# Kernel tuning notes

Hardware: AMD Instinct MI355X
Metric: run time of the kernel (lower is better)

The kernel has to match this reference:

```python
import jax, jax.numpy as jnp
import numpy as np

N, E = 50000, 800000
IN_C, HID, HEADS, OUT_C = 128, 256, 4, 40
C1 = HID // HEADS  # 64 per-head channels in layer 1
NEG_SLOPE = 0.2


def gat_conv(x, edge_index, W, att_src, att_dst, bias, heads, ch, concat):
    """PyG-style GATConv (inference). W:[heads*ch,in], att_*:[heads,ch], bias matches output."""
    n = x.shape[0]
    loop = jnp.arange(n, dtype=edge_index.dtype)
    src = jnp.concatenate([edge_index[0], loop])  # add self-loops (PyG default)
    dst = jnp.concatenate([edge_index[1], loop])
    h = (x @ W.T).reshape(n, heads, ch)                       # [N,H,C]
    a_src = jnp.einsum('nhc,hc->nh', h, att_src)              # [N,H]
    a_dst = jnp.einsum('nhc,hc->nh', h, att_dst)
    logits = jax.nn.leaky_relu(a_src[src] + a_dst[dst], NEG_SLOPE)  # [E',H]
    m = jax.lax.stop_gradient(jax.ops.segment_max(logits, dst, num_segments=n))
    e = jnp.exp(logits - m[dst])
    denom = jax.ops.segment_sum(e, dst, num_segments=n)
    alpha = e / (denom[dst] + 1e-16)                          # [E',H]
    msg = h[src] * alpha[:, :, None]                          # [E',H,C]
    out = jax.ops.segment_sum(msg, dst, num_segments=n)       # [N,H,C]
    out = out.reshape(n, heads * ch) if concat else out.mean(axis=1)
    return out + bias


def setup_inputs() -> dict:
    key = jax.random.key(0)
    ks = jax.random.split(key, 10)
    x = jax.random.normal(ks[0], (N, IN_C), dtype=jnp.float32)
    edge_index = jax.random.randint(ks[1], (2, E), 0, N, dtype=jnp.int64)
    s = 0.1
    W1 = jax.random.normal(ks[2], (HEADS * C1, IN_C), dtype=jnp.float32) * s
    att_src1 = jax.random.normal(ks[3], (HEADS, C1), dtype=jnp.float32) * s
    att_dst1 = jax.random.normal(ks[4], (HEADS, C1), dtype=jnp.float32) * s
    b1 = jnp.zeros((HEADS * C1,), dtype=jnp.float32)
    W2 = jax.random.normal(ks[5], (OUT_C, HID), dtype=jnp.float32) * s
    att_src2 = jax.random.normal(ks[6], (1, OUT_C), dtype=jnp.float32) * s
    att_dst2 = jax.random.normal(ks[7], (1, OUT_C), dtype=jnp.float32) * s
    b2 = jnp.zeros((OUT_C,), dtype=jnp.float32)
    return {"x": x, "edge_index": edge_index, "W1": W1, "att_src1": att_src1,
            "att_dst1": att_dst1, "b1": b1, "W2": W2, "att_src2": att_src2,
            "att_dst2": att_dst2, "b2": b2}


def reference(x, edge_index, W1, att_src1, att_dst1, b1, W2, att_src2, att_dst2, b2):
    h = gat_conv(x, edge_index, W1, att_src1, att_dst1, b1, HEADS, C1, True)
    h = jax.nn.elu(h)
    out = gat_conv(h, edge_index, W2, att_src2, att_dst2, b2, 1, OUT_C, False)
    return out
```

## Files before the change

kernel.cpp:

```cpp
#include <hip/hip_runtime.h>
#include <hip/hip_bf16.h>
#include <cstdint>
#include <cstddef>

#define NN 50000
#define NE 800000
#define INC 128
#define HIDC 256
#define NH 4
#define OUTC 40

#define GE_BLOCKS ((NE + 255)/256)
#define CVT_BLOCKS ((HIDC*INC/4 + 255)/256)
#define G1_BLOCKS ((NN + 63)/64)

typedef __attribute__((ext_vector_type(8))) short short8_t;
typedef __attribute__((ext_vector_type(4))) float f32x4_t;

__device__ __forceinline__ float lrelu(float x){ return x > 0.f ? x : 0.2f*x; }
__device__ __forceinline__ unsigned short bfr(float f){
  __hip_bfloat16 h = __float2bfloat16(f);
  return *reinterpret_cast<unsigned short*>(&h);
}
__device__ __forceinline__ float bflo(unsigned u){ return __uint_as_float(u << 16); }
__device__ __forceinline__ float bfhi(unsigned u){ return __uint_as_float(u & 0xffff0000u); }

__device__ __forceinline__ int probe_flag(const void* ei, int tid, int* sflag){
  if (tid < 64){
    long long v = ((const long long*)ei)[(long long)tid * (NE/64)];
    bool ok = (v >= 0) && (v < NN);
    unsigned long long m = __ballot(ok);
    if (tid == 0) *sflag = (m == 0xFFFFFFFFFFFFFFFFull) ? 1 : 0;
  }
  __syncthreads();
  return *sflag;
}

__global__ __launch_bounds__(256) void k_count_cvt(const void* __restrict__ ei, int* __restrict__ deg,
                                                   const float* __restrict__ W1, unsigned short* __restrict__ w1b){
  int tid = threadIdx.x;
  if (blockIdx.x < CVT_BLOCKS){
    int i = blockIdx.x*256 + tid;
    if (i < HIDC*INC/4){
      float4 v = ((const float4*)W1)[i];
      ushort4 o;
      o.x = bfr(v.x); o.y = bfr(v.y); o.z = bfr(v.z); o.w = bfr(v.w);
      ((ushort4*)w1b)[i] = o;
    }
    return;
  }
  __shared__ int sflag;
  int flag = probe_flag(ei, tid, &sflag);
  int e = (blockIdx.x - CVT_BLOCKS)*256 + tid;
  if (e >= NE) return;
  int d;
  if (flag) d = (int)((const long long*)ei)[NE+e];
  else      d = ((const int*)ei)[NE+e];
  d = min(max(d,0),NN-1);
  atomicAdd(&deg[d], 1);
}

__global__ __launch_bounds__(1024) void k_scan1(const int* __restrict__ deg, int* __restrict__ rowptr, int* __restrict__ sums){
  __shared__ int sh[1024];
  int t = threadIdx.x; int i = blockIdx.x*1024 + t;
  sh[t] = (i < NN) ? deg[i] : 0;
  __syncthreads();
  for (int off = 1; off < 1024; off <<= 1){
    int add = (t >= off) ? sh[t-off] : 0;
    __syncthreads();
    sh[t] += add;
    __syncthreads();
  }
  if (i < NN) rowptr[i+1] = sh[t];
  if (t == 1023) sums[blockIdx.x] = sh[1023];
}

__global__ __launch_bounds__(256) void k_scan3(int* __restrict__ rowptr, const int* __restrict__ sums, int nchunks){
  __shared__ int spre[64];
  int t = threadIdx.x;
  if (t == 0){
    int acc = 0;
    for (int c = 0; c < nchunks; c++){ spre[c] = acc; acc += sums[c]; }
  }
  __syncthreads();
  int i = blockIdx.x*256 + t;
  if (i < NN) rowptr[i+1] += spre[i >> 10];
  if (i == 0) rowptr[0] = 0;
}

__global__ __launch_bounds__(256) void k_gemm1_fill(const float* __restrict__ x, const unsigned short* __restrict__ w1b,
    const float* __restrict__ atts, const float* __restrict__ attd,
    unsigned short* __restrict__ h1b, float* __restrict__ as1, float* __restrict__ ad1,
    const void* __restrict__ ei, const int* __restrict__ rowptr, int* __restrict__ fillc,
    int* __restrict__ colsrc){
  int tid = threadIdx.x;
  if (blockIdx.x < G1_BLOCKS){
    int wv = tid >> 6, l = tid & 63;
    int m0 = blockIdx.x*64 + wv*16;
    int lr = l & 15;
    int lk = l >> 4;

    short8_t a[4];
    int arow = m0 + lr; if (arow > NN-1) arow = NN-1;
    const float* xrow = x + (size_t)arow*INC + lk*8;
    #pragma unroll
    for (int kt = 0; kt < 4; kt++){
      float4 f0 = *(const float4*)(xrow + kt*32);
      float4 f1 = *(const float4*)(xrow + kt*32 + 4);
      short8_t av;
      av[0] = (short)bfr(f0.x); av[1] = (short)bfr(f0.y);
      av[2] = (short)bfr(f0.z); av[3] = (short)bfr(f0.w);
      av[4] = (short)bfr(f1.x); av[5] = (short)bfr(f1.y);
      av[6] = (short)bfr(f1.z); av[7] = (short)bfr(f1.w);
      a[kt] = av;
    }

    const unsigned short* bbase = w1b + (size_t)lr*INC + lk*8;

    for (int h = 0; h < NH; h++){
      float ps[4] = {0.f,0.f,0.f,0.f};
      float pd[4] = {0.f,0.f,0.f,0.f};
      #pragma unroll
      for (int t4 = 0; t4 < 4; t4++){
        int nt = h*4 + t4;
        f32x4_t acc = {0.f,0.f,0.f,0.f};
        #pragma unroll
        for (int kt = 0; kt < 4; kt++){
          short8_t bv = *(const short8_t*)(bbase + (size_t)nt*16*INC + kt*32);
          acc = __builtin_amdgcn_mfma_f32_16x16x32_bf16(a[kt], bv, acc, 0, 0, 0);
        }
        float sa = atts[nt*16 + lr], sd = attd[nt*16 + lr];
        #pragma unroll
        for (int r = 0; r < 4; r++){
          float v = acc[r];
          ps[r] += v*sa; pd[r] += v*sd;
          int node = m0 + lk*4 + r;
          if (node < NN) h1b[(size_t)node*HIDC + nt*16 + lr] = bfr(v);
        }
      }
      #pragma unroll
      for (int r = 0; r < 4; r++){
        float p = ps[r], q = pd[r];
        p += __shfl_xor(p, 1); p += __shfl_xor(p, 2); p += __shfl_xor(p, 4); p += __shfl_xor(p, 8);
        q += __shfl_xor(q, 1); q += __shfl_xor(q, 2); q += __shfl_xor(q, 4); q += __shfl_xor(q, 8);
        int node = m0 + lk*4 + r;
        if (lr == 0 && node < NN){ as1[node*NH + h] = p; ad1[node*NH + h] = q; }
      }
    }
    return;
  }
  __shared__ int sflag;
  int flag = probe_flag(ei, tid, &sflag);
  int e = (blockIdx.x - G1_BLOCKS)*256 + tid;
  if (e >= NE) return;
  int s, d;
  if (flag){
    const long long* p = (const long long*)ei;
    s = (int)p[e]; d = (int)p[NE+e];
  } else {
    const int* p = (const int*)ei;
    s = p[e]; d = p[NE+e];
  }
  s = min(max(s,0),NN-1); d = min(max(d,0),NN-1);
  int pos = rowptr[d] + atomicAdd(&fillc[d], 1);
  colsrc[pos] = s;
}

__global__ __launch_bounds__(128) void k_agg1(const unsigned short* __restrict__ h1b,
    const float* __restrict__ as1, const float* __restrict__ ad1,
    const int* __restrict__ colsrc, const int* __restrict__ rowptr,
    const float* __restrict__ b1, unsigned short* __restrict__ h1a){
  int n = blockIdx.x*2 + (threadIdx.x >> 6);
  if (n >= NN) return;
  int tid = threadIdx.x & 63;
  int head = tid >> 4;
  const uint2* h1q = (const uint2*)h1b;

  float adn = ad1[n*NH + head];
  float es_self = __expf(lrelu(as1[n*NH + head] + adn));
  float den = 1e-16f + es_self;
  uint2 v = h1q[(size_t)n*64 + tid];
  float a0 = es_self * bflo(v.x);
  float a1 = es_self * bfhi(v.x);
  float a2 = es_self * bflo(v.y);
  float a3 = es_self * bfhi(v.y);

  int beg = rowptr[n], end = rowptr[n+1];
  int j = beg;
  for (; j + 7 < end; j += 8){
    int s[8]; float w[8]; uint2 g[8];
    #pragma unroll
    for (int u = 0; u < 8; u++) s[u] = colsrc[j+u];
    #pragma unroll
    for (int u = 0; u < 8; u++) g[u] = h1q[(size_t)s[u]*64 + tid];
    #pragma unroll
    for (int u = 0; u < 8; u++) w[u] = as1[s[u]*NH + head];
    #pragma unroll
    for (int u = 0; u < 8; u++) w[u] = __expf(lrelu(w[u] + adn));
    #pragma unroll
    for (int u = 0; u < 8; u++){
      den += w[u];
      a0 += w[u]*bflo(g[u].x); a1 += w[u]*bfhi(g[u].x);
      a2 += w[u]*bflo(g[u].y); a3 += w[u]*bfhi(g[u].y);
    }
  }
  for (; j + 3 < end; j += 4){
    int s[4]; float w[4]; uint2 g[4];
    #pragma unroll
    for (int u = 0; u < 4; u++) s[u] = colsrc[j+u];
    #pragma unroll
    for (int u = 0; u < 4; u++) g[u] = h1q[(size_t)s[u]*64 + tid];
    #pragma unroll
    for (int u = 0; u < 4; u++) w[u] = __expf(lrelu(as1[s[u]*NH + head] + adn));
    #pragma unroll
    for (int u = 0; u < 4; u++){
      den += w[u];
      a0 += w[u]*bflo(g[u].x); a1 += w[u]*bfhi(g[u].x);
      a2 += w[u]*bflo(g[u].y); a3 += w[u]*bfhi(g[u].y);
    }
  }
  for (; j < end; j++){
    int s0 = colsrc[j];
    uint2 g0 = h1q[(size_t)s0*64 + tid];
    float w0 = __expf(lrelu(as1[s0*NH + head] + adn));
    den += w0;
    a0 += w0*bflo(g0.x); a1 += w0*bfhi(g0.x); a2 += w0*bflo(g0.y); a3 += w0*bfhi(g0.y);
  }

  float4 bb = ((const float4*)b1)[tid];
  float rinv = 1.f / den;
  float o0 = a0*rinv + bb.x;
  float o1 = a1*rinv + bb.y;
  float o2 = a2*rinv + bb.z;
  float o3 = a3*rinv + bb.w;
  o0 = o0 > 0.f ? o0 : (__expf(o0) - 1.f);
  o1 = o1 > 0.f ? o1 : (__expf(o1) - 1.f);
  o2 = o2 > 0.f ? o2 : (__expf(o2) - 1.f);
  o3 = o3 > 0.f ? o3 : (__expf(o3) - 1.f);
  uint2 pkd;
  pkd.x = (unsigned)bfr(o0) | ((unsigned)bfr(o1) << 16);
  pkd.y = (unsigned)bfr(o2) | ((unsigned)bfr(o3) << 16);
  ((uint2*)h1a)[(size_t)n*64 + tid] = pkd;
}

__global__ __launch_bounds__(128) void k_gemm2(const unsigned short* __restrict__ h1a, const float* __restrict__ W2,
    const float* __restrict__ atts2, const float* __restrict__ attd2,
    unsigned* __restrict__ h2b, float* __restrict__ a2s, float* __restrict__ a2d){
  __shared__ float W2t[HIDC*OUTC];
  __shared__ float sA[OUTC], sD[OUTC];
  int tid = threadIdx.x;
  #pragma unroll
  for (int it = 0; it < (OUTC*HIDC)/128; it++){
    int idx = it*128 + tid;
    int c = idx >> 8, k = idx & 255;
    W2t[k*OUTC + c] = W2[idx];
  }
  if (tid < OUTC){ sA[tid] = atts2[tid]; sD[tid] = attd2[tid]; }
  __syncthreads();

  int n = blockIdx.x*128 + tid;
  if (n >= NN) return;

  float acc[OUTC];
  #pragma unroll
  for (int c = 0; c < OUTC; c++) acc[c] = 0.f;

  const uint2* x2p = (const uint2*)(h1a + (size_t)n*HIDC);
  const float4* w4p = (const float4*)W2t;
  #pragma unroll 2
  for (int k4 = 0; k4 < HIDC/4; k4++){
    uint2 xu = x2p[k4];
    float xk[4] = { bflo(xu.x), bfhi(xu.x), bflo(xu.y), bfhi(xu.y) };
    #pragma unroll
    for (int kk = 0; kk < 4; kk++){
      #pragma unroll
      for (int c4 = 0; c4 < OUTC/4; c4++){
        float4 wv = w4p[(k4*4 + kk)*(OUTC/4) + c4];
        acc[c4*4+0] += xk[kk]*wv.x;
        acc[c4*4+1] += xk[kk]*wv.y;
        acc[c4*4+2] += xk[kk]*wv.z;
        acc[c4*4+3] += xk[kk]*wv.w;
      }
    }
  }

  float s2 = 0.f, d2 = 0.f;
  #pragma unroll
  for (int c = 0; c < OUTC; c++){ s2 += acc[c]*sA[c]; d2 += acc[c]*sD[c]; }

  unsigned* h2row = h2b + (size_t)n*(OUTC/2);
  #pragma unroll
  for (int c2 = 0; c2 < OUTC/2; c2++)
    h2row[c2] = (unsigned)bfr(acc[c2*2]) | ((unsigned)bfr(acc[c2*2+1]) << 16);
  a2s[n] = s2; a2d[n] = d2;
}

__global__ __launch_bounds__(128) void k_agg2(const unsigned* __restrict__ h2b, const float* __restrict__ a2s,
    const float* __restrict__ a2d, const int* __restrict__ colsrc, const int* __restrict__ rowptr,
    const float* __restrict__ b2, float* __restrict__ out){
  int tid = threadIdx.x & 63;
  int half = threadIdx.x >> 6;
  int sub = tid / 20, c2 = tid % 20;
  int n = blockIdx.x*6 + half*3 + sub;
  bool valid = (sub < 3) && (n < NN);
  int nn = valid ? n : 0;

  float a2dn = a2d[nn];
  float e = __expf(lrelu(a2s[nn] + a2dn));
  float den = 1e-16f + e;
  unsigned v = h2b[(size_t)nn*20 + c2];
  float acc0 = e * bflo(v);
  float acc1 = e * bfhi(v);

  int beg = valid ? rowptr[nn] : 0;
  int end = valid ? rowptr[nn+1] : 0;
  int j = beg;
  for (; j + 7 < end; j += 8){
    int s[8]; float w[8]; unsigned g[8];
    #pragma unroll
    for (int u = 0; u < 8; u++) s[u] = colsrc[j+u];
    #pragma unroll
    for (int u = 0; u < 8; u++) g[u] = h2b[(size_t)s[u]*20 + c2];
    #pragma unroll
    for (int u = 0; u < 8; u++) w[u] = a2s[s[u]];
    #pragma unroll
    for (int u = 0; u < 8; u++) w[u] = __expf(lrelu(w[u] + a2dn));
    #pragma unroll
    for (int u = 0; u < 8; u++){
      den += w[u];
      acc0 += w[u]*bflo(g[u]);
      acc1 += w[u]*bfhi(g[u]);
    }
  }
  for (; j + 3 < end; j += 4){
    int s[4]; float w[4]; unsigned g[4];
    #pragma unroll
    for (int u = 0; u < 4; u++) s[u] = colsrc[j+u];
    #pragma unroll
    for (int u = 0; u < 4; u++) g[u] = h2b[(size_t)s[u]*20 + c2];
    #pragma unroll
    for (int u = 0; u < 4; u++) w[u] = __expf(lrelu(a2s[s[u]] + a2dn));
    #pragma unroll
    for (int u = 0; u < 4; u++){
      den += w[u];
      acc0 += w[u]*bflo(g[u]);
      acc1 += w[u]*bfhi(g[u]);
    }
  }
  for (; j < end; j++){
    int s0 = colsrc[j];
    unsigned g0 = h2b[(size_t)s0*20 + c2];
    float w0 = __expf(lrelu(a2s[s0] + a2dn));
    den += w0;
    acc0 += w0*bflo(g0);
    acc1 += w0*bfhi(g0);
  }

  if (valid){
    float rinv = 1.f / den;
    float2 o;
    o.x = acc0*rinv + b2[c2*2];
    o.y = acc1*rinv + b2[c2*2+1];
    ((float2*)(out + (size_t)n*OUTC))[c2] = o;
  }
}

extern "C" void kernel_launch(void* const* d_in, const int* in_sizes, int n_in,
                              void* d_out, int out_size, void* d_ws, size_t ws_size,
                              hipStream_t stream){
  const float* x    = (const float*)d_in[0];
  const void*  ei   = d_in[1];
  const float* W1   = (const float*)d_in[2];
  const float* as1w = (const float*)d_in[3];
  const float* ad1w = (const float*)d_in[4];
  const float* b1   = (const float*)d_in[5];
  const float* W2   = (const float*)d_in[6];
  const float* as2w = (const float*)d_in[7];
  const float* ad2w = (const float*)d_in[8];
  const float* b2   = (const float*)d_in[9];
  float* out = (float*)d_out;

  char* base = (char*)d_ws;
  size_t off = 0;
  auto alloc = [&](size_t bytes)->char*{ char* r = base + off; off += (bytes + 255) & ~(size_t)255; return r; };
  int* deg    = (int*)alloc((size_t)NN*sizeof(int));
  int* rowptr = (int*)alloc((size_t)(NN+1)*sizeof(int));
  int* fillc  = (int*)alloc((size_t)NN*sizeof(int));
  int* sums   = (int*)alloc(64*sizeof(int));
  int* colsrc = (int*)alloc((size_t)NE*sizeof(int));
  unsigned short* w1b = (unsigned short*)alloc((size_t)HIDC*INC*sizeof(unsigned short));
  unsigned short* h1b = (unsigned short*)alloc((size_t)NN*HIDC*sizeof(unsigned short));
  unsigned short* h1a = (unsigned short*)alloc((size_t)NN*HIDC*sizeof(unsigned short));
  float* as1  = (float*)alloc((size_t)NN*NH*sizeof(float));
  float* ad1  = (float*)alloc((size_t)NN*NH*sizeof(float));
  unsigned* h2b = (unsigned*)alloc((size_t)NN*(OUTC/2)*sizeof(unsigned));
  float* a2s  = (float*)alloc((size_t)NN*sizeof(float));
  float* a2d  = (float*)alloc((size_t)NN*sizeof(float));

  hipMemsetAsync(deg,   0, (size_t)NN*sizeof(int), stream);
  hipMemsetAsync(fillc, 0, (size_t)NN*sizeof(int), stream);

  int nchunks = (NN + 1023)/1024;
  k_count_cvt<<<CVT_BLOCKS + GE_BLOCKS, 256, 0, stream>>>(ei, deg, W1, w1b);
  k_scan1<<<nchunks, 1024, 0, stream>>>(deg, rowptr, sums);
  k_scan3<<<(NN + 255)/256, 256, 0, stream>>>(rowptr, sums, nchunks);
  k_gemm1_fill<<<G1_BLOCKS + GE_BLOCKS, 256, 0, stream>>>(x, w1b, as1w, ad1w, h1b, as1, ad1,
                                                          ei, rowptr, fillc, colsrc);
  k_agg1<<<(NN + 1)/2, 128, 0, stream>>>(h1b, as1, ad1, colsrc, rowptr, b1, h1a);
  k_gemm2<<<(NN + 127)/128, 128, 0, stream>>>(h1a, W2, as2w, ad2w, h2b, a2s, a2d);
  k_agg2<<<(NN + 5)/6, 128, 0, stream>>>(h2b, a2s, a2d, colsrc, rowptr, b2, out);
}
```

Before: 230.9 us.

## Split hidden features into 32-channel planes and slice aggregation across blocks

```diff
diff --git a/kernel.cpp b/kernel.cpp
--- a/kernel.cpp
+++ b/kernel.cpp
@@ -75,7 +75,8 @@
   if (t == 1023) sums[blockIdx.x] = sh[1023];
 }
 
-__global__ __launch_bounds__(256) void k_scan3(int* __restrict__ rowptr, const int* __restrict__ sums, int nchunks){
+__global__ __launch_bounds__(256) void k_scan3(int* __restrict__ rowptr, const int* __restrict__ sums, int nchunks,
+                                               int* __restrict__ fillc){
   __shared__ int spre[64];
   int t = threadIdx.x;
   if (t == 0){
@@ -84,13 +85,13 @@
   }
   __syncthreads();
   int i = blockIdx.x*256 + t;
-  if (i < NN) rowptr[i+1] += spre[i >> 10];
+  if (i < NN){ rowptr[i+1] += spre[i >> 10]; fillc[i] = 0; }
   if (i == 0) rowptr[0] = 0;
 }
 
 __global__ __launch_bounds__(256) void k_gemm1_fill(const float* __restrict__ x, const unsigned short* __restrict__ w1b,
     const float* __restrict__ atts, const float* __restrict__ attd,
-    unsigned short* __restrict__ h1b, float* __restrict__ as1, float* __restrict__ ad1,
+    unsigned short* __restrict__ h1p, float* __restrict__ as1, float* __restrict__ ad1,
     const void* __restrict__ ei, const int* __restrict__ rowptr, int* __restrict__ fillc,
     int* __restrict__ colsrc){
   int tid = threadIdx.x;
@@ -129,13 +130,15 @@
           short8_t bv = *(const short8_t*)(bbase + (size_t)nt*16*INC + kt*32);
           acc = __builtin_amdgcn_mfma_f32_16x16x32_bf16(a[kt], bv, acc, 0, 0, 0);
         }
-        float sa = atts[nt*16 + lr], sd = attd[nt*16 + lr];
+        int col = nt*16 + lr;
+        int plane = col >> 5, within = col & 31;
+        float sa = atts[col], sd = attd[col];
         #pragma unroll
         for (int r = 0; r < 4; r++){
           float v = acc[r];
           ps[r] += v*sa; pd[r] += v*sd;
           int node = m0 + lk*4 + r;
-          if (node < NN) h1b[(size_t)node*HIDC + nt*16 + lr] = bfr(v);
+          if (node < NN) h1p[(size_t)plane*NN*32 + (size_t)node*32 + within] = bfr(v);
         }
       }
       #pragma unroll
@@ -166,20 +169,23 @@
   colsrc[pos] = s;
 }
 
-__global__ __launch_bounds__(128) void k_agg1(const unsigned short* __restrict__ h1b,
+__global__ __launch_bounds__(128) void k_agg1(const unsigned short* __restrict__ h1p,
     const float* __restrict__ as1, const float* __restrict__ ad1,
     const int* __restrict__ colsrc, const int* __restrict__ rowptr,
     const float* __restrict__ b1, unsigned short* __restrict__ h1a){
-  int n = blockIdx.x*2 + (threadIdx.x >> 6);
+  int slice = blockIdx.x & 7;
+  int grp = blockIdx.x >> 3;
+  int n = grp*16 + (threadIdx.x >> 3);
   if (n >= NN) return;
-  int tid = threadIdx.x & 63;
-  int head = tid >> 4;
-  const uint2* h1q = (const uint2*)h1b;
+  int li = threadIdx.x & 7;
+  int head = slice >> 1;
+
+  const uint2* hp = (const uint2*)h1p + (size_t)slice*NN*8;
 
   float adn = ad1[n*NH + head];
   float es_self = __expf(lrelu(as1[n*NH + head] + adn));
   float den = 1e-16f + es_self;
-  uint2 v = h1q[(size_t)n*64 + tid];
+  uint2 v = hp[(size_t)n*8 + li];
   float a0 = es_self * bflo(v.x);
   float a1 = es_self * bfhi(v.x);
   float a2 = es_self * bflo(v.y);
@@ -187,31 +193,16 @@
 
   int beg = rowptr[n], end = rowptr[n+1];
   int j = beg;
-  for (; j + 7 < end; j += 8){
-    int s[8]; float w[8]; uint2 g[8];
-    #pragma unroll
-    for (int u = 0; u < 8; u++) s[u] = colsrc[j+u];
-    #pragma unroll
-    for (int u = 0; u < 8; u++) g[u] = h1q[(size_t)s[u]*64 + tid];
-    #pragma unroll
-    for (int u = 0; u < 8; u++) w[u] = as1[s[u]*NH + head];
-    #pragma unroll
-    for (int u = 0; u < 8; u++) w[u] = __expf(lrelu(w[u] + adn));
-    #pragma unroll
-    for (int u = 0; u < 8; u++){
-      den += w[u];
-      a0 += w[u]*bflo(g[u].x); a1 += w[u]*bfhi(g[u].x);
-      a2 += w[u]*bflo(g[u].y); a3 += w[u]*bfhi(g[u].y);
-    }
-  }
   for (; j + 3 < end; j += 4){
     int s[4]; float w[4]; uint2 g[4];
     #pragma unroll
     for (int u = 0; u < 4; u++) s[u] = colsrc[j+u];
     #pragma unroll
-    for (int u = 0; u < 4; u++) g[u] = h1q[(size_t)s[u]*64 + tid];
-    #pragma unroll
-    for (int u = 0; u < 4; u++) w[u] = __expf(lrelu(as1[s[u]*NH + head] + adn));
+    for (int u = 0; u < 4; u++) g[u] = hp[(size_t)s[u]*8 + li];
+    #pragma unroll
+    for (int u = 0; u < 4; u++) w[u] = as1[s[u]*NH + head];
+    #pragma unroll
+    for (int u = 0; u < 4; u++) w[u] = __expf(lrelu(w[u] + adn));
     #pragma unroll
     for (int u = 0; u < 4; u++){
       den += w[u];
@@ -221,13 +212,13 @@
   }
   for (; j < end; j++){
     int s0 = colsrc[j];
-    uint2 g0 = h1q[(size_t)s0*64 + tid];
+    uint2 g0 = hp[(size_t)s0*8 + li];
     float w0 = __expf(lrelu(as1[s0*NH + head] + adn));
     den += w0;
     a0 += w0*bflo(g0.x); a1 += w0*bfhi(g0.x); a2 += w0*bflo(g0.y); a3 += w0*bfhi(g0.y);
   }
 
-  float4 bb = ((const float4*)b1)[tid];
+  float4 bb = ((const float4*)b1)[slice*8 + li];
   float rinv = 1.f / den;
   float o0 = a0*rinv + bb.x;
   float o1 = a1*rinv + bb.y;
@@ -240,7 +231,7 @@
   uint2 pkd;
   pkd.x = (unsigned)bfr(o0) | ((unsigned)bfr(o1) << 16);
   pkd.y = (unsigned)bfr(o2) | ((unsigned)bfr(o3) << 16);
-  ((uint2*)h1a)[(size_t)n*64 + tid] = pkd;
+  ((uint2*)h1a)[(size_t)slice*NN*8 + (size_t)n*8 + li] = pkd;
 }
 
 __global__ __launch_bounds__(128) void k_gemm2(const unsigned short* __restrict__ h1a, const float* __restrict__ W2,
@@ -265,21 +256,26 @@
   #pragma unroll
   for (int c = 0; c < OUTC; c++) acc[c] = 0.f;
 
-  const uint2* x2p = (const uint2*)(h1a + (size_t)n*HIDC);
+  const uint2* h1a2 = (const uint2*)h1a;
   const float4* w4p = (const float4*)W2t;
-  #pragma unroll 2
-  for (int k4 = 0; k4 < HIDC/4; k4++){
-    uint2 xu = x2p[k4];
-    float xk[4] = { bflo(xu.x), bfhi(xu.x), bflo(xu.y), bfhi(xu.y) };
-    #pragma unroll
-    for (int kk = 0; kk < 4; kk++){
+  #pragma unroll
+  for (int p = 0; p < 8; p++){
+    const uint2* xp = h1a2 + (size_t)p*NN*8 + (size_t)n*8;
+    #pragma unroll 2
+    for (int q = 0; q < 8; q++){
+      uint2 xu = xp[q];
+      float xk[4] = { bflo(xu.x), bfhi(xu.x), bflo(xu.y), bfhi(xu.y) };
+      int kbase = p*32 + q*4;
       #pragma unroll
-      for (int c4 = 0; c4 < OUTC/4; c4++){
-        float4 wv = w4p[(k4*4 + kk)*(OUTC/4) + c4];
-        acc[c4*4+0] += xk[kk]*wv.x;
-        acc[c4*4+1] += xk[kk]*wv.y;
-        acc[c4*4+2] += xk[kk]*wv.z;
-        acc[c4*4+3] += xk[kk]*wv.w;
+      for (int kk = 0; kk < 4; kk++){
+        #pragma unroll
+        for (int c4 = 0; c4 < OUTC/4; c4++){
+          float4 wv = w4p[(kbase + kk)*(OUTC/4) + c4];
+          acc[c4*4+0] += xk[kk]*wv.x;
+          acc[c4*4+1] += xk[kk]*wv.y;
+          acc[c4*4+2] += xk[kk]*wv.z;
+          acc[c4*4+3] += xk[kk]*wv.w;
+        }
       }
     }
   }
@@ -298,70 +294,60 @@
 __global__ __launch_bounds__(128) void k_agg2(const unsigned* __restrict__ h2b, const float* __restrict__ a2s,
     const float* __restrict__ a2d, const int* __restrict__ colsrc, const int* __restrict__ rowptr,
     const float* __restrict__ b2, float* __restrict__ out){
-  int tid = threadIdx.x & 63;
-  int half = threadIdx.x >> 6;
-  int sub = tid / 20, c2 = tid % 20;
-  int n = blockIdx.x*6 + half*3 + sub;
-  bool valid = (sub < 3) && (n < NN);
+  int lane = threadIdx.x & 63;
+  int wave = threadIdx.x >> 6;
+  int sub = lane / 10, li = lane % 10;
+  int n = blockIdx.x*12 + wave*6 + sub;
+  bool valid = (sub < 6) && (n < NN);
   int nn = valid ? n : 0;
+  const uint2* h2q = (const uint2*)h2b;
 
   float a2dn = a2d[nn];
   float e = __expf(lrelu(a2s[nn] + a2dn));
   float den = 1e-16f + e;
-  unsigned v = h2b[(size_t)nn*20 + c2];
-  float acc0 = e * bflo(v);
-  float acc1 = e * bfhi(v);
+  uint2 v = h2q[(size_t)nn*10 + li];
+  float c0 = e * bflo(v.x);
+  float c1 = e * bfhi(v.x);
+  float c2 = e * bflo(v.y);
+  float c3 = e * bfhi(v.y);
 
   int beg = valid ? rowptr[nn] : 0;
   int end = valid ? rowptr[nn+1] : 0;
   int j = beg;
-  for (; j + 7 < end; j += 8){
-    int s[8]; float w[8]; unsigned g[8];
-    #pragma unroll
-    for (int u = 0; u < 8; u++) s[u] = colsrc[j+u];
-    #pragma unroll
-    for (int u = 0; u < 8; u++) g[u] = h2b[(size_t)s[u]*20 + c2];
-    #pragma unroll
-    for (int u = 0; u < 8; u++) w[u] = a2s[s[u]];
-    #pragma unroll
-    for (int u = 0; u < 8; u++) w[u] = __expf(lrelu(w[u] + a2dn));
-    #pragma unroll
-    for (int u = 0; u < 8; u++){
-      den += w[u];
-      acc0 += w[u]*bflo(g[u]);
-      acc1 += w[u]*bfhi(g[u]);
-    }
-  }
   for (; j + 3 < end; j += 4){
-    int s[4]; float w[4]; unsigned g[4];
+    int s[4]; float w[4]; uint2 g[4];
     #pragma unroll
     for (int u = 0; u < 4; u++) s[u] = colsrc[j+u];
     #pragma unroll
-    for (int u = 0; u < 4; u++) g[u] = h2b[(size_t)s[u]*20 + c2];
-    #pragma unroll
-    for (int u = 0; u < 4; u++) w[u] = __expf(lrelu(a2s[s[u]] + a2dn));
+    for (int u = 0; u < 4; u++) g[u] = h2q[(size_t)s[u]*10 + li];
+    #pragma unroll
+    for (int u = 0; u < 4; u++) w[u] = a2s[s[u]];
+    #pragma unroll
+    for (int u = 0; u < 4; u++) w[u] = __expf(lrelu(w[u] + a2dn));
     #pragma unroll
     for (int u = 0; u < 4; u++){
       den += w[u];
-      acc0 += w[u]*bflo(g[u]);
-      acc1 += w[u]*bfhi(g[u]);
+      c0 += w[u]*bflo(g[u].x); c1 += w[u]*bfhi(g[u].x);
+      c2 += w[u]*bflo(g[u].y); c3 += w[u]*bfhi(g[u].y);
     }
   }
   for (; j < end; j++){
     int s0 = colsrc[j];
-    unsigned g0 = h2b[(size_t)s0*20 + c2];
+    uint2 g0 = h2q[(size_t)s0*10 + li];
     float w0 = __expf(lrelu(a2s[s0] + a2dn));
     den += w0;
-    acc0 += w0*bflo(g0);
-    acc1 += w0*bfhi(g0);
+    c0 += w0*bflo(g0.x); c1 += w0*bfhi(g0.x); c2 += w0*bflo(g0.y); c3 += w0*bfhi(g0.y);
   }
 
   if (valid){
     float rinv = 1.f / den;
-    float2 o;
-    o.x = acc0*rinv + b2[c2*2];
-    o.y = acc1*rinv + b2[c2*2+1];
-    ((float2*)(out + (size_t)n*OUTC))[c2] = o;
+    float4 bb = ((const float4*)b2)[li];
+    float4 o;
+    o.x = c0*rinv + bb.x;
+    o.y = c1*rinv + bb.y;
+    o.z = c2*rinv + bb.z;
+    o.w = c3*rinv + bb.w;
+    ((float4*)(out + (size_t)n*OUTC))[li] = o;
   }
 }
 
@@ -389,7 +375,7 @@
   int* sums   = (int*)alloc(64*sizeof(int));
   int* colsrc = (int*)alloc((size_t)NE*sizeof(int));
   unsigned short* w1b = (unsigned short*)alloc((size_t)HIDC*INC*sizeof(unsigned short));
-  unsigned short* h1b = (unsigned short*)alloc((size_t)NN*HIDC*sizeof(unsigned short));
+  unsigned short* h1p = (unsigned short*)alloc((size_t)NN*HIDC*sizeof(unsigned short));
   unsigned short* h1a = (unsigned short*)alloc((size_t)NN*HIDC*sizeof(unsigned short));
   float* as1  = (float*)alloc((size_t)NN*NH*sizeof(float));
   float* ad1  = (float*)alloc((size_t)NN*NH*sizeof(float));
@@ -397,16 +383,15 @@
   float* a2s  = (float*)alloc((size_t)NN*sizeof(float));
   float* a2d  = (float*)alloc((size_t)NN*sizeof(float));
 
-  hipMemsetAsync(deg,   0, (size_t)NN*sizeof(int), stream);
-  hipMemsetAsync(fillc, 0, (size_t)NN*sizeof(int), stream);
+  hipMemsetAsync(deg, 0, (size_t)NN*sizeof(int), stream);
 
   int nchunks = (NN + 1023)/1024;
   k_count_cvt<<<CVT_BLOCKS + GE_BLOCKS, 256, 0, stream>>>(ei, deg, W1, w1b);
   k_scan1<<<nchunks, 1024, 0, stream>>>(deg, rowptr, sums);
-  k_scan3<<<(NN + 255)/256, 256, 0, stream>>>(rowptr, sums, nchunks);
-  k_gemm1_fill<<<G1_BLOCKS + GE_BLOCKS, 256, 0, stream>>>(x, w1b, as1w, ad1w, h1b, as1, ad1,
+  k_scan3<<<(NN + 255)/256, 256, 0, stream>>>(rowptr, sums, nchunks, fillc);
+  k_gemm1_fill<<<G1_BLOCKS + GE_BLOCKS, 256, 0, stream>>>(x, w1b, as1w, ad1w, h1p, as1, ad1,
                                                           ei, rowptr, fillc, colsrc);
-  k_agg1<<<(NN + 1)/2, 128, 0, stream>>>(h1b, as1, ad1, colsrc, rowptr, b1, h1a);
+  k_agg1<<<8 * ((NN + 15)/16), 128, 0, stream>>>(h1p, as1, ad1, colsrc, rowptr, b1, h1a);
   k_gemm2<<<(NN + 127)/128, 128, 0, stream>>>(h1a, W2, as2w, ad2w, h2b, a2s, a2d);
-  k_agg2<<<(NN + 5)/6, 128, 0, stream>>>(h2b, a2s, a2d, colsrc, rowptr, b2, out);
-}
+  k_agg2<<<(NN + 11)/12, 128, 0, stream>>>(h2b, a2s, a2d, colsrc, rowptr, b2, out);
+}
```

Measured after the change: 249.0 us. +7.8%, slower.
